# Kernel optimization log

Hardware: AMD Instinct MI355X
Metric: run time of the kernel (lower is better)

Reference implementation:

```python
import jax, jax.numpy as jnp
import numpy as np


def setup_inputs() -> dict:
    key = jax.random.key(0)
    k_x, k_b = jax.random.split(key)
    B, C, H, W = 32, 512, 32, 32
    x = jax.random.normal(k_x, (B, C, H, W), dtype=jnp.float32)
    beta = jax.random.normal(k_b, (1,), dtype=jnp.float32)
    return {"x": x, "beta": beta}


def reference(x, beta):
    B, C, H, W = x.shape
    feat = x.reshape(B, C, H * W)                       # [B, C, N]
    # channel-channel Gram matrix: [B, C, C]
    attn = jnp.einsum('bcn,bdn->bcd', feat, feat)
    # DANet-style reversed scores: rowmax - score, then softmax over last dim
    attn = jnp.max(attn, axis=-1, keepdims=True) - attn
    attn = jax.nn.softmax(attn, axis=-1)
    feat_e = jnp.einsum('bcd,bdn->bcn', attn, feat).reshape(B, C, H, W)
    return beta * feat_e + x
```

## Files before the change

### kernel.cpp

```cpp
#include <hip/hip_runtime.h>
#include <math.h>

constexpr int B = 32, C = 512, N = 1024;

typedef float f32x4 __attribute__((ext_vector_type(4)));
typedef _Float16 f16x8 __attribute__((ext_vector_type(8)));
typedef unsigned short u16x4 __attribute__((ext_vector_type(4)));

__device__ __forceinline__ unsigned short f32_to_f16u(float v) {
  union { _Float16 h; unsigned short u; } cv; cv.h = (_Float16)v; return cv.u;
}
__device__ __forceinline__ float f16u_to_f32(unsigned short u) {
  union { _Float16 h; unsigned short u; } cv; cv.u = u; return (float)cv.h;
}

__device__ __forceinline__ void glds16(const void* g, void* l) {
  __builtin_amdgcn_global_load_lds((const __attribute__((address_space(1))) void*)g,
                                   (__attribute__((address_space(3))) void*)l, 16, 0, 0);
}

__global__ __launch_bounds__(256) void convert_kernel(const float* __restrict__ x,
                                                      unsigned short* __restrict__ xf,
                                                      unsigned short* __restrict__ xlo,
                                                      unsigned short* __restrict__ xfT) {
  const int b = blockIdx.z;
  const int cy = blockIdx.y * 64;
  const int nx = blockIdx.x * 64;
  const int t = threadIdx.x;
  const int r = t >> 4, c4 = (t & 15) * 4;

  __shared__ unsigned T[64][65];

#pragma unroll
  for (int rr = 0; rr < 64; rr += 16) {
    const int row = rr + r;
    const size_t gi = ((size_t)b * C + cy + row) * N + nx + c4;
    const float4 v = *(const float4*)&x[gi];
    u16x4 h, l;
    h[0] = f32_to_f16u(v.x); l[0] = f32_to_f16u((v.x - f16u_to_f32(h[0])) * 2048.0f);
    h[1] = f32_to_f16u(v.y); l[1] = f32_to_f16u((v.y - f16u_to_f32(h[1])) * 2048.0f);
    h[2] = f32_to_f16u(v.z); l[2] = f32_to_f16u((v.z - f16u_to_f32(h[2])) * 2048.0f);
    h[3] = f32_to_f16u(v.w); l[3] = f32_to_f16u((v.w - f16u_to_f32(h[3])) * 2048.0f);
    *(u16x4*)&xf[gi]  = h;
    *(u16x4*)&xlo[gi] = l;
    T[row][c4 + 0] = h[0]; T[row][c4 + 1] = h[1];
    T[row][c4 + 2] = h[2]; T[row][c4 + 3] = h[3];
  }
  __syncthreads();
#pragma unroll
  for (int rr = 0; rr < 64; rr += 16) {
    const int nrow = rr + r;
    u16x4 o;
    o[0] = (unsigned short)T[c4 + 0][nrow]; o[1] = (unsigned short)T[c4 + 1][nrow];
    o[2] = (unsigned short)T[c4 + 2][nrow]; o[3] = (unsigned short)T[c4 + 3][nrow];
    *(u16x4*)&xfT[((size_t)b * N + nx + nrow) * C + cy + c4] = o;
  }
}

__global__ __launch_bounds__(512, 2) void gram_soft(const unsigned short* __restrict__ xf,
                                                    const unsigned short* __restrict__ xlo,
                                                    unsigned short* __restrict__ Af) {
  const int l = blockIdx.x;
  const int xcd = l & 7, seq = l >> 3;
  const int b = xcd + 8 * (seq >> 3);
  const int i0 = (seq & 7) * 64;

  const unsigned short* __restrict__ Fh = xf  + (size_t)b * C * N;
  const unsigned short* __restrict__ Fl = xlo + (size_t)b * C * N;
  unsigned short* __restrict__ Ab = Af + (size_t)b * C * C;

  __shared__ __align__(16) unsigned short P[2][512 * 32];

  const int t = threadIdx.x, wave = t >> 6, lane = t & 63;
  const int lrow = lane & 15, quad = lane >> 4;
  const int srow = lane >> 2;
  const int sel  = ((lane & 3) ^ ((lane >> 3) & 3)) * 8;
  const int fsw  = (lrow >> 1) & 3;

  f32x4 acc[4][4] = {};
  f32x4 acl[4][4] = {};

#define STAGE(k0, nb)                                                     \
  {                                                                       \
    _Pragma("unroll")                                                     \
    for (int cc = 0; cc < 4; ++cc) {                                      \
      const int chunk = wave * 4 + cc;                                    \
      const int row = chunk * 16 + srow;                                  \
      glds16(Fh + (size_t)row * N + (k0) + sel, &P[nb][chunk * 512]);     \
    }                                                                     \
  }

  STAGE(0, 0);

  f16x8 alc[4];
#pragma unroll
  for (int ti = 0; ti < 4; ++ti)
    alc[ti] = *(const f16x8*)&Fl[(size_t)(i0 + ti * 16 + lrow) * N + quad * 8];

  for (int it = 0; it < 32; ++it) {
    const int k0 = it * 32;
    __syncthreads();
    if (it + 1 < 32) STAGE(k0 + 32, (it + 1) & 1);

    f16x8 aln[4];
    if (it + 1 < 32) {
#pragma unroll
      for (int ti = 0; ti < 4; ++ti)
        aln[ti] = *(const f16x8*)&Fl[(size_t)(i0 + ti * 16 + lrow) * N + k0 + 32 + quad * 8];
    }

    const unsigned short* __restrict__ Pc = P[it & 1];
    f16x8 ah[4], bh[4];
#pragma unroll
    for (int ti = 0; ti < 4; ++ti) {
      const int r = i0 + ti * 16 + lrow;
      ah[ti] = *(const f16x8*)&Pc[r * 32 + (quad ^ fsw) * 8];
    }
#pragma unroll
    for (int tj = 0; tj < 4; ++tj) {
      const int r = wave * 64 + tj * 16 + lrow;
      bh[tj] = *(const f16x8*)&Pc[r * 32 + (quad ^ fsw) * 8];
    }
#pragma unroll
    for (int ti = 0; ti < 4; ++ti)
#pragma unroll
      for (int tj = 0; tj < 4; ++tj) {
        acc[ti][tj] = __builtin_amdgcn_mfma_f32_16x16x32_f16(ah[ti],  bh[tj], acc[ti][tj], 0, 0, 0);
        acl[ti][tj] = __builtin_amdgcn_mfma_f32_16x16x32_f16(alc[ti], bh[tj], acl[ti][tj], 0, 0, 0);
      }
    if (it + 1 < 32) {
#pragma unroll
      for (int ti = 0; ti < 4; ++ti) alc[ti] = aln[ti];
    }
  }
#undef STAGE

#pragma unroll
  for (int ti = 0; ti < 4; ++ti)
#pragma unroll
    for (int tj = 0; tj < 4; ++tj)
#pragma unroll
      for (int r = 0; r < 4; ++r)
        acc[ti][tj][r] = fmaf(acl[ti][tj][r], 4.8828125e-4f, acc[ti][tj][r]);

  __syncthreads();
  float* red = (float*)&P[0][0];
  float* fin = (float*)&P[1][0];

  float m[16];
#pragma unroll
  for (int ti = 0; ti < 4; ++ti)
#pragma unroll
    for (int r = 0; r < 4; ++r)
      m[ti * 4 + r] = fminf(fminf(acc[ti][0][r], acc[ti][1][r]),
                            fminf(acc[ti][2][r], acc[ti][3][r]));
#pragma unroll
  for (int o = 1; o < 16; o <<= 1)
#pragma unroll
    for (int s = 0; s < 16; ++s) m[s] = fminf(m[s], __shfl_xor(m[s], o, 64));
  if (lrow == 0)
#pragma unroll
    for (int ti = 0; ti < 4; ++ti)
#pragma unroll
      for (int r = 0; r < 4; ++r)
        red[wave * 64 + ti * 16 + quad * 4 + r] = m[ti * 4 + r];
  __syncthreads();
  if (t < 64) {
    float v = red[t];
#pragma unroll
    for (int w = 1; w < 8; ++w) v = fminf(v, red[w * 64 + t]);
    fin[t] = v;
  }
  __syncthreads();

  float sm[16];
#pragma unroll
  for (int ti = 0; ti < 4; ++ti)
#pragma unroll
    for (int r = 0; r < 4; ++r) {
      const float mn = fin[ti * 16 + quad * 4 + r];
      float s = 0.f;
#pragma unroll
      for (int tj = 0; tj < 4; ++tj) {
        const float e = __expf(mn - acc[ti][tj][r]);
        acc[ti][tj][r] = e;
        s += e;
      }
      sm[ti * 4 + r] = s;
    }
#pragma unroll
  for (int o = 1; o < 16; o <<= 1)
#pragma unroll
    for (int s = 0; s < 16; ++s) sm[s] += __shfl_xor(sm[s], o, 64);
  if (lrow == 0)
#pragma unroll
    for (int ti = 0; ti < 4; ++ti)
#pragma unroll
      for (int r = 0; r < 4; ++r)
        red[wave * 64 + ti * 16 + quad * 4 + r] = sm[ti * 4 + r];
  __syncthreads();
  if (t < 64) {
    float v = 0.f;
#pragma unroll
    for (int w = 0; w < 8; ++w) v += red[w * 64 + t];
    fin[t] = 1.0f / v;
  }
  __syncthreads();

#pragma unroll
  for (int ti = 0; ti < 4; ++ti)
#pragma unroll
    for (int r = 0; r < 4; ++r) {
      const float inv = fin[ti * 16 + quad * 4 + r];
      const int grow = i0 + ti * 16 + quad * 4 + r;
#pragma unroll
      for (int tj = 0; tj < 4; ++tj) {
        const int gcol = wave * 64 + tj * 16 + lrow;
        Ab[(size_t)grow * C + gcol] = f32_to_f16u(acc[ti][tj][r] * inv);
      }
    }
}

__global__ __launch_bounds__(256, 4) void av_mfma(const unsigned short* __restrict__ Af,
                                                  const unsigned short* __restrict__ xfT,
                                                  const float* __restrict__ x,
                                                  const float* __restrict__ beta,
                                                  float* __restrict__ out) {
  const int l = blockIdx.x;
  const int xcd = l & 7, seq = l >> 3;
  const int b = xcd + 8 * (seq >> 5);
  const int tile = seq & 31;
  const int i0 = (tile >> 3) * 128;
  const int j0 = (tile & 7) * 128;

  const unsigned short* __restrict__ Ab = Af  + (size_t)b * C * C;
  const unsigned short* __restrict__ FT = xfT + (size_t)b * N * C;
  const float* __restrict__ xb = x + (size_t)b * C * N;
  float* __restrict__ ob = out + (size_t)b * C * N;

  __shared__ __align__(16) unsigned short SMEM[2 * 128 * 64];
  unsigned short* As = SMEM;
  unsigned short* Bs = SMEM + 128 * 64;

  const int t = threadIdx.x, wave = t >> 6, lane = t & 63;
  const int wi = wave >> 1, wj = wave & 1;
  const int lrow = lane & 15, quad = lane >> 4;
  const int srow8 = lane >> 3;
  const int sel = ((lane & 7) ^ srow8) * 8;

  f32x4 acc[4][4] = {};

  for (int k0 = 0; k0 < C; k0 += 64) {
    __syncthreads();
#pragma unroll
    for (int cc = 0; cc < 4; ++cc) {
      const int chunk = wave * 4 + cc;
      const int row = chunk * 8 + srow8;
      glds16(Ab + (size_t)(i0 + row) * C + k0 + sel, &As[chunk * 512]);
      glds16(FT + (size_t)(j0 + row) * C + k0 + sel, &Bs[chunk * 512]);
    }
    __syncthreads();

#pragma unroll
    for (int kh = 0; kh < 2; ++kh) {
      f16x8 af[4], bf[4];
#pragma unroll
      for (int ti = 0; ti < 4; ++ti) {
        const int r = wi * 64 + ti * 16 + lrow;
        af[ti] = *(const f16x8*)&As[r * 64 + ((kh * 4 + quad) ^ (r & 7)) * 8];
      }
#pragma unroll
      for (int tj = 0; tj < 4; ++tj) {
        const int r = wj * 64 + tj * 16 + lrow;
        bf[tj] = *(const f16x8*)&Bs[r * 64 + ((kh * 4 + quad) ^ (r & 7)) * 8];
      }
#pragma unroll
      for (int ti = 0; ti < 4; ++ti)
#pragma unroll
        for (int tj = 0; tj < 4; ++tj)
          acc[ti][tj] = __builtin_amdgcn_mfma_f32_16x16x32_f16(af[ti], bf[tj], acc[ti][tj], 0, 0, 0);
    }
  }

  __syncthreads();
  float* fs = (float*)SMEM + wave * 1024;
  const float bv = beta[0];
#pragma unroll
  for (int ti = 0; ti < 4; ++ti) {
#pragma unroll
    for (int tj = 0; tj < 4; ++tj)
#pragma unroll
      for (int r = 0; r < 4; ++r)
        fs[(quad * 4 + r) * 64 + tj * 16 + lrow] = acc[ti][tj][r];
    __syncthreads();
#pragma unroll
    for (int p = 0; p < 4; ++p) {
      const int f = p * 64 + lane;
      const int rr = f >> 4, cc4 = (f & 15) * 4;
      const f32x4 e = *(const f32x4*)&fs[rr * 64 + cc4];
      const int gr = i0 + wi * 64 + ti * 16 + rr;
      const int gc = j0 + wj * 64 + cc4;
      const size_t o = (size_t)gr * N + gc;
      const float4 xv = *(const float4*)&xb[o];
      float4 ov;
      ov.x = fmaf(bv, e[0], xv.x);
      ov.y = fmaf(bv, e[1], xv.y);
      ov.z = fmaf(bv, e[2], xv.z);
      ov.w = fmaf(bv, e[3], xv.w);
      *(float4*)&ob[o] = ov;
    }
    __syncthreads();
  }
}

extern "C" void kernel_launch(void* const* d_in, const int* in_sizes, int n_in,
                              void* d_out, int out_size, void* d_ws, size_t ws_size,
                              hipStream_t stream) {
  const float* x    = (const float*)d_in[0];
  const float* beta = (const float*)d_in[1];
  float* out = (float*)d_out;

  char* ws = (char*)d_ws;
  unsigned short* xf  = (unsigned short*)ws; ws += (size_t)B * C * N * 2;
  unsigned short* xlo = (unsigned short*)ws; ws += (size_t)B * C * N * 2;
  unsigned short* xfT = (unsigned short*)ws; ws += (size_t)B * N * C * 2;
  unsigned short* Af  = (unsigned short*)ws;

  convert_kernel<<<dim3(N / 64, C / 64, B), dim3(256), 0, stream>>>(x, xf, xlo, xfT);
  gram_soft     <<<dim3(256),               dim3(512), 0, stream>>>(xf, xlo, Af);
  av_mfma       <<<dim3(1024),              dim3(256), 0, stream>>>(Af, xfT, x, beta, out);
}
```

Before: 210.7 us.

## Drop fp16 residual-split compensation and read residual from fp16 copy

Removes the low-order fp16 residual term, so the Gram matrix is computed from a single fp16 product. This halves the MFMA work in gram_soft and removes the xlo buffer and its writes and reads. gram_soft is retiled to 1024 threads (16 waves in a 2x8 grid). The final residual add reads the fp16 copy of x instead of fp32 x and uses nontemporal stores for the output. The cost is lower accuracy: both the attention logits and the residual term carry fp16 rounding error.

```diff
diff --git a/kernel.cpp b/kernel.cpp
--- a/kernel.cpp
+++ b/kernel.cpp
@@ -21,7 +21,6 @@
 
 __global__ __launch_bounds__(256) void convert_kernel(const float* __restrict__ x,
                                                       unsigned short* __restrict__ xf,
-                                                      unsigned short* __restrict__ xlo,
                                                       unsigned short* __restrict__ xfT) {
   const int b = blockIdx.z;
   const int cy = blockIdx.y * 64;
@@ -36,13 +35,10 @@
     const int row = rr + r;
     const size_t gi = ((size_t)b * C + cy + row) * N + nx + c4;
     const float4 v = *(const float4*)&x[gi];
-    u16x4 h, l;
-    h[0] = f32_to_f16u(v.x); l[0] = f32_to_f16u((v.x - f16u_to_f32(h[0])) * 2048.0f);
-    h[1] = f32_to_f16u(v.y); l[1] = f32_to_f16u((v.y - f16u_to_f32(h[1])) * 2048.0f);
-    h[2] = f32_to_f16u(v.z); l[2] = f32_to_f16u((v.z - f16u_to_f32(h[2])) * 2048.0f);
-    h[3] = f32_to_f16u(v.w); l[3] = f32_to_f16u((v.w - f16u_to_f32(h[3])) * 2048.0f);
-    *(u16x4*)&xf[gi]  = h;
-    *(u16x4*)&xlo[gi] = l;
+    u16x4 h;
+    h[0] = f32_to_f16u(v.x); h[1] = f32_to_f16u(v.y);
+    h[2] = f32_to_f16u(v.z); h[3] = f32_to_f16u(v.w);
+    *(u16x4*)&xf[gi] = h;
     T[row][c4 + 0] = h[0]; T[row][c4 + 1] = h[1];
     T[row][c4 + 2] = h[2]; T[row][c4 + 3] = h[3];
   }
@@ -57,34 +53,32 @@
   }
 }
 
-__global__ __launch_bounds__(512, 2) void gram_soft(const unsigned short* __restrict__ xf,
-                                                    const unsigned short* __restrict__ xlo,
-                                                    unsigned short* __restrict__ Af) {
+__global__ __launch_bounds__(1024, 4) void gram_soft(const unsigned short* __restrict__ xf,
+                                                     unsigned short* __restrict__ Af) {
   const int l = blockIdx.x;
   const int xcd = l & 7, seq = l >> 3;
   const int b = xcd + 8 * (seq >> 3);
   const int i0 = (seq & 7) * 64;
 
-  const unsigned short* __restrict__ Fh = xf  + (size_t)b * C * N;
-  const unsigned short* __restrict__ Fl = xlo + (size_t)b * C * N;
+  const unsigned short* __restrict__ Fh = xf + (size_t)b * C * N;
   unsigned short* __restrict__ Ab = Af + (size_t)b * C * C;
 
   __shared__ __align__(16) unsigned short P[2][512 * 32];
 
   const int t = threadIdx.x, wave = t >> 6, lane = t & 63;
+  const int wi = wave >> 3;
+  const int wj = wave & 7;
   const int lrow = lane & 15, quad = lane >> 4;
   const int srow = lane >> 2;
   const int sel  = ((lane & 3) ^ ((lane >> 3) & 3)) * 8;
-  const int fsw  = (lrow >> 1) & 3;
-
-  f32x4 acc[4][4] = {};
-  f32x4 acl[4][4] = {};
+
+  f32x4 acc[2][4] = {};
 
 #define STAGE(k0, nb)                                                     \
   {                                                                       \
     _Pragma("unroll")                                                     \
-    for (int cc = 0; cc < 4; ++cc) {                                      \
-      const int chunk = wave * 4 + cc;                                    \
+    for (int cc = 0; cc < 2; ++cc) {                                      \
+      const int chunk = wave * 2 + cc;                                    \
       const int row = chunk * 16 + srow;                                  \
       glds16(Fh + (size_t)row * N + (k0) + sel, &P[nb][chunk * 512]);     \
     }                                                                     \
@@ -92,138 +86,114 @@
 
   STAGE(0, 0);
 
-  f16x8 alc[4];
-#pragma unroll
-  for (int ti = 0; ti < 4; ++ti)
-    alc[ti] = *(const f16x8*)&Fl[(size_t)(i0 + ti * 16 + lrow) * N + quad * 8];
-
   for (int it = 0; it < 32; ++it) {
     const int k0 = it * 32;
     __syncthreads();
     if (it + 1 < 32) STAGE(k0 + 32, (it + 1) & 1);
 
-    f16x8 aln[4];
-    if (it + 1 < 32) {
-#pragma unroll
-      for (int ti = 0; ti < 4; ++ti)
-        aln[ti] = *(const f16x8*)&Fl[(size_t)(i0 + ti * 16 + lrow) * N + k0 + 32 + quad * 8];
-    }
-
     const unsigned short* __restrict__ Pc = P[it & 1];
-    f16x8 ah[4], bh[4];
-#pragma unroll
-    for (int ti = 0; ti < 4; ++ti) {
-      const int r = i0 + ti * 16 + lrow;
-      ah[ti] = *(const f16x8*)&Pc[r * 32 + (quad ^ fsw) * 8];
+    f16x8 ah[2], bh[4];
+#pragma unroll
+    for (int ti = 0; ti < 2; ++ti) {
+      const int r = i0 + wi * 32 + ti * 16 + lrow;
+      ah[ti] = *(const f16x8*)&Pc[r * 32 + (quad ^ ((r >> 1) & 3)) * 8];
     }
 #pragma unroll
     for (int tj = 0; tj < 4; ++tj) {
-      const int r = wave * 64 + tj * 16 + lrow;
-      bh[tj] = *(const f16x8*)&Pc[r * 32 + (quad ^ fsw) * 8];
-    }
-#pragma unroll
-    for (int ti = 0; ti < 4; ++ti)
+      const int r = wj * 64 + tj * 16 + lrow;
+      bh[tj] = *(const f16x8*)&Pc[r * 32 + (quad ^ ((r >> 1) & 3)) * 8];
+    }
+#pragma unroll
+    for (int ti = 0; ti < 2; ++ti)
+#pragma unroll
+      for (int tj = 0; tj < 4; ++tj)
+        acc[ti][tj] = __builtin_amdgcn_mfma_f32_16x16x32_f16(ah[ti], bh[tj], acc[ti][tj], 0, 0, 0);
+  }
+#undef STAGE
+
+  __syncthreads();
+  float* red = (float*)&P[0][0];
+  float* fin = red + 512;
+
+  float m[8];
+#pragma unroll
+  for (int ti = 0; ti < 2; ++ti)
+#pragma unroll
+    for (int rr = 0; rr < 4; ++rr)
+      m[ti * 4 + rr] = fminf(fminf(acc[ti][0][rr], acc[ti][1][rr]),
+                             fminf(acc[ti][2][rr], acc[ti][3][rr]));
+#pragma unroll
+  for (int o = 1; o < 16; o <<= 1)
+#pragma unroll
+    for (int s = 0; s < 8; ++s) m[s] = fminf(m[s], __shfl_xor(m[s], o, 64));
+  if (lrow == 0)
+#pragma unroll
+    for (int ti = 0; ti < 2; ++ti)
+#pragma unroll
+      for (int rr = 0; rr < 4; ++rr)
+        red[wave * 32 + ti * 16 + quad * 4 + rr] = m[ti * 4 + rr];
+  __syncthreads();
+  if (t < 64) {
+    const int wig = t >> 5, loc = t & 31;
+    float v = red[(wig * 8) * 32 + loc];
+#pragma unroll
+    for (int j = 1; j < 8; ++j) v = fminf(v, red[(wig * 8 + j) * 32 + loc]);
+    fin[t] = v;
+  }
+  __syncthreads();
+
+  float sm[8];
+#pragma unroll
+  for (int ti = 0; ti < 2; ++ti)
+#pragma unroll
+    for (int rr = 0; rr < 4; ++rr) {
+      const float mn = fin[wi * 32 + ti * 16 + quad * 4 + rr];
+      float s = 0.f;
 #pragma unroll
       for (int tj = 0; tj < 4; ++tj) {
-        acc[ti][tj] = __builtin_amdgcn_mfma_f32_16x16x32_f16(ah[ti],  bh[tj], acc[ti][tj], 0, 0, 0);
-        acl[ti][tj] = __builtin_amdgcn_mfma_f32_16x16x32_f16(alc[ti], bh[tj], acl[ti][tj], 0, 0, 0);
-      }
-    if (it + 1 < 32) {
-#pragma unroll
-      for (int ti = 0; ti < 4; ++ti) alc[ti] = aln[ti];
-    }
-  }
-#undef STAGE
-
-#pragma unroll
-  for (int ti = 0; ti < 4; ++ti)
-#pragma unroll
-    for (int tj = 0; tj < 4; ++tj)
-#pragma unroll
-      for (int r = 0; r < 4; ++r)
-        acc[ti][tj][r] = fmaf(acl[ti][tj][r], 4.8828125e-4f, acc[ti][tj][r]);
-
-  __syncthreads();
-  float* red = (float*)&P[0][0];
-  float* fin = (float*)&P[1][0];
-
-  float m[16];
-#pragma unroll
-  for (int ti = 0; ti < 4; ++ti)
-#pragma unroll
-    for (int r = 0; r < 4; ++r)
-      m[ti * 4 + r] = fminf(fminf(acc[ti][0][r], acc[ti][1][r]),
-                            fminf(acc[ti][2][r], acc[ti][3][r]));
-#pragma unroll
-  for (int o = 1; o < 16; o <<= 1)
-#pragma unroll
-    for (int s = 0; s < 16; ++s) m[s] = fminf(m[s], __shfl_xor(m[s], o, 64));
-  if (lrow == 0)
-#pragma unroll
-    for (int ti = 0; ti < 4; ++ti)
-#pragma unroll
-      for (int r = 0; r < 4; ++r)
-        red[wave * 64 + ti * 16 + quad * 4 + r] = m[ti * 4 + r];
-  __syncthreads();
-  if (t < 64) {
-    float v = red[t];
-#pragma unroll
-    for (int w = 1; w < 8; ++w) v = fminf(v, red[w * 64 + t]);
-    fin[t] = v;
-  }
-  __syncthreads();
-
-  float sm[16];
-#pragma unroll
-  for (int ti = 0; ti < 4; ++ti)
-#pragma unroll
-    for (int r = 0; r < 4; ++r) {
-      const float mn = fin[ti * 16 + quad * 4 + r];
-      float s = 0.f;
-#pragma unroll
-      for (int tj = 0; tj < 4; ++tj) {
-        const float e = __expf(mn - acc[ti][tj][r]);
-        acc[ti][tj][r] = e;
+        const float e = __expf(mn - acc[ti][tj][rr]);
+        acc[ti][tj][rr] = e;
         s += e;
       }
-      sm[ti * 4 + r] = s;
+      sm[ti * 4 + rr] = s;
     }
 #pragma unroll
   for (int o = 1; o < 16; o <<= 1)
 #pragma unroll
-    for (int s = 0; s < 16; ++s) sm[s] += __shfl_xor(sm[s], o, 64);
+    for (int s = 0; s < 8; ++s) sm[s] += __shfl_xor(sm[s], o, 64);
   if (lrow == 0)
 #pragma unroll
-    for (int ti = 0; ti < 4; ++ti)
-#pragma unroll
-      for (int r = 0; r < 4; ++r)
-        red[wave * 64 + ti * 16 + quad * 4 + r] = sm[ti * 4 + r];
+    for (int ti = 0; ti < 2; ++ti)
+#pragma unroll
+      for (int rr = 0; rr < 4; ++rr)
+        red[wave * 32 + ti * 16 + quad * 4 + rr] = sm[ti * 4 + rr];
   __syncthreads();
   if (t < 64) {
+    const int wig = t >> 5, loc = t & 31;
     float v = 0.f;
 #pragma unroll
-    for (int w = 0; w < 8; ++w) v += red[w * 64 + t];
+    for (int j = 0; j < 8; ++j) v += red[(wig * 8 + j) * 32 + loc];
     fin[t] = 1.0f / v;
   }
   __syncthreads();
 
 #pragma unroll
-  for (int ti = 0; ti < 4; ++ti)
-#pragma unroll
-    for (int r = 0; r < 4; ++r) {
-      const float inv = fin[ti * 16 + quad * 4 + r];
-      const int grow = i0 + ti * 16 + quad * 4 + r;
+  for (int ti = 0; ti < 2; ++ti)
+#pragma unroll
+    for (int rr = 0; rr < 4; ++rr) {
+      const float inv = fin[wi * 32 + ti * 16 + quad * 4 + rr];
+      const int grow = i0 + wi * 32 + ti * 16 + quad * 4 + rr;
 #pragma unroll
       for (int tj = 0; tj < 4; ++tj) {
-        const int gcol = wave * 64 + tj * 16 + lrow;
-        Ab[(size_t)grow * C + gcol] = f32_to_f16u(acc[ti][tj][r] * inv);
+        const int gcol = wj * 64 + tj * 16 + lrow;
+        Ab[(size_t)grow * C + gcol] = f32_to_f16u(acc[ti][tj][rr] * inv);
       }
     }
 }
 
 __global__ __launch_bounds__(256, 4) void av_mfma(const unsigned short* __restrict__ Af,
                                                   const unsigned short* __restrict__ xfT,
-                                                  const float* __restrict__ x,
+                                                  const unsigned short* __restrict__ xf,
                                                   const float* __restrict__ beta,
                                                   float* __restrict__ out) {
   const int l = blockIdx.x;
@@ -235,7 +205,7 @@
 
   const unsigned short* __restrict__ Ab = Af  + (size_t)b * C * C;
   const unsigned short* __restrict__ FT = xfT + (size_t)b * N * C;
-  const float* __restrict__ xb = x + (size_t)b * C * N;
+  const unsigned short* __restrict__ xb = xf  + (size_t)b * C * N;
   float* __restrict__ ob = out + (size_t)b * C * N;
 
   __shared__ __align__(16) unsigned short SMEM[2 * 128 * 64];
@@ -301,13 +271,13 @@
       const int gr = i0 + wi * 64 + ti * 16 + rr;
       const int gc = j0 + wj * 64 + cc4;
       const size_t o = (size_t)gr * N + gc;
-      const float4 xv = *(const float4*)&xb[o];
-      float4 ov;
-      ov.x = fmaf(bv, e[0], xv.x);
-      ov.y = fmaf(bv, e[1], xv.y);
-      ov.z = fmaf(bv, e[2], xv.z);
-      ov.w = fmaf(bv, e[3], xv.w);
-      *(float4*)&ob[o] = ov;
+      const u16x4 xv = *(const u16x4*)&xb[o];
+      f32x4 ov;
+      ov[0] = fmaf(bv, e[0], f16u_to_f32(xv[0]));
+      ov[1] = fmaf(bv, e[1], f16u_to_f32(xv[1]));
+      ov[2] = fmaf(bv, e[2], f16u_to_f32(xv[2]));
+      ov[3] = fmaf(bv, e[3], f16u_to_f32(xv[3]));
+      __builtin_nontemporal_store(ov, (f32x4*)&ob[o]);
     }
     __syncthreads();
   }
@@ -322,11 +292,10 @@
 
   char* ws = (char*)d_ws;
   unsigned short* xf  = (unsigned short*)ws; ws += (size_t)B * C * N * 2;
-  unsigned short* xlo = (unsigned short*)ws; ws += (size_t)B * C * N * 2;
   unsigned short* xfT = (unsigned short*)ws; ws += (size_t)B * N * C * 2;
   unsigned short* Af  = (unsigned short*)ws;
 
-  convert_kernel<<<dim3(N / 64, C / 64, B), dim3(256), 0, stream>>>(x, xf, xlo, xfT);
-  gram_soft     <<<dim3(256),               dim3(512), 0, stream>>>(xf, xlo, Af);
-  av_mfma       <<<dim3(1024),              dim3(256), 0, stream>>>(Af, xfT, x, beta, out);
-}
+  convert_kernel<<<dim3(N / 64, C / 64, B), dim3(256),  0, stream>>>(x, xf, xfT);
+  gram_soft     <<<dim3(256),               dim3(1024), 0, stream>>>(xf, Af);
+  av_mfma       <<<dim3(1024),              dim3(256),  0, stream>>>(Af, xfT, xf, beta, out);
+}
```

Result: faster. 174.9 us (-17.0%).
